# Kernel tuning notes

Measured on AMD Instinct MI355X. Metric: run time of the kernel, lower is better.

The kernel has to match this reference:

```python
import jax, jax.numpy as jnp
import numpy as np

K = 3       # kernel_size
STRIDE = 1


def setup_inputs() -> dict:
    key = jax.random.key(0)
    k1, k2, k3 = jax.random.split(key, 3)
    B, C, H, W = 128, 64, 32, 32
    O = 64
    OH = (H - K) // STRIDE + 1  # 30
    OW = (W - K) // STRIDE + 1  # 30
    x = jax.random.normal(k1, (B, C, H, W), dtype=jnp.float32)
    weight = jax.random.normal(k2, (O, C, OH, OW, K, K), dtype=jnp.float32)
    bias = jax.random.normal(k3, (O, OH, OW), dtype=jnp.float32)
    return {"x": x, "weight": weight, "bias": bias}


def reference(x, weight, bias):
    # x: [B, C, H, W]; weight: [O, C, OH, OW, K, K]; bias: [O, OH, OW]
    O, C, OH, OW, _, _ = weight.shape
    # Extract all k x k patches in one pass: [B, C*K*K, OH, OW],
    # feature axis ordered (C, kh, kw) with spatial fastest.
    patches = jax.lax.conv_general_dilated_patches(
        x, filter_shape=(K, K), window_strides=(STRIDE, STRIDE), padding="VALID"
    )
    # Faithful to torch einsum 'bcih,coih->bo': the region's channel axis is
    # contracted against the weight's FIRST axis (nominal out_channels), and the
    # output channel is the weight's SECOND axis (requires C == O).
    # Rearrange weight -> [C*K*K (contract), O (output), OH, OW].
    w = jnp.transpose(weight, (0, 4, 5, 1, 2, 3)).reshape(C * K * K, O, OH, OW)
    out = jnp.einsum("bpij,poij->boij", patches, w) + bias[None]
    return out  # [B, O, OH, OW]
```

## Files before the change

### kernel.cpp

```cpp
#include <hip/hip_runtime.h>


typedef __bf16 bf16x8 __attribute__((ext_vector_type(8)));
typedef float f32x4 __attribute__((ext_vector_type(4)));
typedef unsigned long long u64;
typedef unsigned int u32t;
typedef unsigned short u16t;

struct __attribute__((packed, aligned(8))) uf4 { f32x4 v; };
struct __attribute__((packed, aligned(8))) uf2 { float2 v; };
struct __attribute__((packed, aligned(4))) uq2 { u64 x, y; };
struct __attribute__((aligned(16))) ull2 { u64 x, y; };

__device__ __forceinline__ u16t f2bf(float f) {
  union { float f; u32t u; } v; v.f = f;
  u32t r = v.u + 0x7fffu + ((v.u >> 16) & 1u);
  return (u16t)(r >> 16);
}
__device__ __forceinline__ u32t pk2(float a, float b) {
  return (u32t)f2bf(a) | ((u32t)f2bf(b) << 16);
}
__device__ __forceinline__ u64 pk3(float a, float b, float c) {
  return (u64)f2bf(a) | ((u64)f2bf(b) << 16) | ((u64)f2bf(c) << 32);
}
__device__ __forceinline__ bf16x8 mk_af(u64 lo, u64 hi) {
  union { u64 q[2]; bf16x8 v; } u;
  u.q[0] = lo; u.q[1] = hi;
  return u.v;
}


__global__ __launch_bounds__(256) void lcl_prep_x(const float* __restrict__ x,
                                                  u16t* __restrict__ Xb) {
  int gid = blockIdx.x * 256 + threadIdx.x;
  int b  = gid & 127;
  int ch = gid >> 7;
  const float* src = x + (size_t)b * 65536 + ch * 32;
  u16t* dst = Xb + (size_t)gid * 32;
  u64 qv[8];
#pragma unroll
  for (int s = 0; s < 8; ++s) {
    f32x4 a = ((const uf4*)(src + s * 4))->v;
    qv[s] = (u64)pk2(a[0], a[1]) | ((u64)pk2(a[2], a[3]) << 32);
  }
#pragma unroll
  for (int s = 0; s < 4; ++s) {
    ull2 w; w.x = qv[2 * s]; w.y = qv[2 * s + 1];
    *(ull2*)(dst + s * 8) = w;
  }
}

__global__ __launch_bounds__(256, 2) void lcl_main(
    const u16t* __restrict__ Xb, const float* __restrict__ wgt,
    const float* __restrict__ bias, float* __restrict__ out) {
  int bid = blockIdx.x;
  int xcd = bid & 7, sg = bid >> 3;
  int t = xcd * 75 + sg;
  int jg = t % 5;
  int r  = t / 5;
  int bg = r & 1, og = (r >> 1) & 1, i = r >> 2;
  int j0 = jg * 6;
  int ij0 = i * 30 + j0;

  __shared__ __align__(16) u16t Bt[2 * 6 * 32 * 104];

  const int tid  = threadIdx.x;
  const int wave = tid >> 6;
  const int lane = tid & 63;
  const int lrow = lane & 15;
  const int q    = lane >> 4;

  const int b_x = bg * 64 + wave * 16 + lrow;
  const char* xbase = (const char*)Xb;
  u32t xoff[3][2];
#pragma unroll
  for (int s = 0; s < 3; ++s)
#pragma unroll
    for (int tt = 0; tt < 2; ++tt) {
      int g = s * 8 + q * 2 + tt, cc = g / 3, kh = g - cc * 3;
      xoff[s][tt] = (u32t)(((cc * 32 + (i + kh)) * 128 + b_x) * 64 + j0 * 2);
    }

  const int ccw = tid >> 5, ow = tid & 31;
  const float* wb = wgt + ((size_t)ccw * 64 + og * 32 + ow) * 8100 + ij0 * 9;

  uq2   rq[3][2];
  f32x4 wv[13];
  float2 wv2;

#define GF(K) ((K) < 52 ? wv[(K) >> 2][(K)&3] : ((K) == 52 ? wv2.x : wv2.y))

#define LOAD_CHUNK(C0)                                                      \
  {                                                                         \
    const size_t xadv = (size_t)(C0) * 262144;                              \
    _Pragma("unroll") for (int s = 0; s < 3; ++s)                           \
    _Pragma("unroll") for (int tt = 0; tt < 2; ++tt)                        \
      rq[s][tt] = *(const uq2*)(xbase + xadv + xoff[s][tt]);                \
    const float* wq = wb + (size_t)(C0) * 518400;                           \
    _Pragma("unroll") for (int e = 0; e < 13; ++e)                          \
      wv[e] = ((const uf4*)(wq + e * 4))->v;                                \
    wv2 = ((const uf2*)(wq + 52))->v;                                       \
  }

  f32x4 acc[6][2];
#pragma unroll
  for (int a = 0; a < 6; ++a)
#pragma unroll
    for (int n = 0; n < 2; ++n) acc[a][n] = f32x4{0.f, 0.f, 0.f, 0.f};

  LOAD_CHUNK(0)

  for (int chunk = 0; chunk < 8; ++chunk) {
    u16t* B = Bt + (chunk & 1) * 19968;

#pragma unroll
    for (int dj = 0; dj < 6; ++dj) {
      u16t* Bp = B + dj * 3328 + ow * 104 + ccw * 12;
#pragma unroll
      for (int kh = 0; kh < 3; ++kh) {
        const int k0 = dj * 9 + kh * 3;
        *(u64*)&Bp[kh * 4] = pk3(GF(k0), GF(k0 + 1), GF(k0 + 2));
      }
    }

    u64 rb[3][2][2];
#pragma unroll
    for (int s = 0; s < 3; ++s)
#pragma unroll
      for (int tt = 0; tt < 2; ++tt) {
        rb[s][tt][0] = rq[s][tt].x;
        rb[s][tt][1] = rq[s][tt].y;
      }

    __syncthreads();

    if (chunk < 7) LOAD_CHUNK((chunk + 1) * 8)

#pragma unroll
    for (int s = 0; s < 3; ++s) {
#pragma unroll
      for (int jj = 0; jj < 6; ++jj) {
        bf16x8 bfr0 = *(const bf16x8*)&B[jj * 3328 + lrow * 104 + s * 32 + q * 8];
        bf16x8 bfr1 = *(const bf16x8*)&B[jj * 3328 + (16 + lrow) * 104 + s * 32 + q * 8];
        u64 lo, hi;
        if (jj == 0) {
          lo = rb[s][0][0];
          hi = rb[s][1][0];
        } else if (jj < 4) {
          lo = (rb[s][0][0] >> (16 * jj)) | (rb[s][0][1] << (64 - 16 * jj));
          hi = (rb[s][1][0] >> (16 * jj)) | (rb[s][1][1] << (64 - 16 * jj));
        } else if (jj == 4) {
          lo = rb[s][0][1];
          hi = rb[s][1][1];
        } else {
          lo = rb[s][0][1] >> 16;
          hi = rb[s][1][1] >> 16;
        }
        bf16x8 af = mk_af(lo, hi);
        acc[jj][0] = __builtin_amdgcn_mfma_f32_16x16x32_bf16(af, bfr0, acc[jj][0], 0, 0, 0);
        acc[jj][1] = __builtin_amdgcn_mfma_f32_16x16x32_bf16(af, bfr1, acc[jj][1], 0, 0, 0);
      }
    }
  }

  const int b0 = bg * 64 + wave * 16 + q * 4;
#pragma unroll
  for (int nt = 0; nt < 2; ++nt) {
    int o = og * 32 + nt * 16 + lrow;
    const float* bp = bias + o * 900 + ij0;
    float2 bv0 = ((const uf2*)bp)->v;
    float2 bv1 = ((const uf2*)(bp + 2))->v;
    float2 bv2 = ((const uf2*)(bp + 4))->v;
#pragma unroll
    for (int rr = 0; rr < 4; ++rr) {
      float* op = out + (size_t)(b0 + rr) * 57600 + o * 900 + ij0;
      float2 r0{acc[0][nt][rr] + bv0.x, acc[1][nt][rr] + bv0.y};
      float2 r1{acc[2][nt][rr] + bv1.x, acc[3][nt][rr] + bv1.y};
      float2 r2{acc[4][nt][rr] + bv2.x, acc[5][nt][rr] + bv2.y};
      ((uf2*)op)->v = r0;
      ((uf2*)(op + 2))->v = r1;
      ((uf2*)(op + 4))->v = r2;
    }
  }
}

__global__ __launch_bounds__(256, 2) void lcl_r4(
    const float* __restrict__ x, const float* __restrict__ wgt,
    const float* __restrict__ bias, float* __restrict__ out) {
  int blk = blockIdx.x;
  int xcd = blk & 7, sg = blk >> 3;
  int t = xcd * 56 + (xcd < 2 ? xcd : 2) + sg;
  int i = t / 15;
  int j0 = (t % 15) * 2;
  int ij0 = i * 30 + j0;

  __shared__ __align__(16) u16t Bt[2 * 2 * 64 * 104];

  const int tid  = threadIdx.x;
  const int wave = tid >> 6;
  const int lane = tid & 63;
  const int lrow = lane & 15;
  const int q    = lane >> 4;

  {
    u64* zp = (u64*)Bt;
#pragma unroll
    for (int k = 0; k < 26; ++k) zp[tid + k * 256] = 0ull;
  }

  int xoffF[3][2];
#pragma unroll
  for (int s = 0; s < 3; ++s)
#pragma unroll
    for (int tt = 0; tt < 2; ++tt) {
      int g = s * 8 + q * 2 + tt, cc = g / 3, kh = g - cc * 3;
      xoffF[s][tt] = cc * 1024 + kh * 32;
    }
  const float* xb0 = x + (wave * 32 + lrow) * 65536 + i * 32 + j0;
  const float* xb1 = xb0 + 16 * 65536;

  const int o_w = tid & 63;
  const float* wb0 = wgt + (size_t)wave * 518400 + o_w * 8100 + ij0 * 9;
  const float* wb1 = wb0 + (size_t)4 * 518400;

  f32x4 av[2][3][2];
  f32x4 wv[2][5];

#define LOAD_CHUNK4(C0)                                                       \
  {                                                                           \
    const float* xc0 = xb0 + (C0) * 1024;                                     \
    const float* xc1 = xb1 + (C0) * 1024;                                     \
    _Pragma("unroll") for (int s = 0; s < 3; ++s)                             \
    _Pragma("unroll") for (int tt = 0; tt < 2; ++tt) {                        \
      av[0][s][tt] = ((const uf4*)(xc0 + xoffF[s][tt]))->v;                   \
      av[1][s][tt] = ((const uf4*)(xc1 + xoffF[s][tt]))->v;                   \
    }                                                                         \
    const float* w0 = wb0 + (size_t)(C0) * 518400;                            \
    const float* w1 = wb1 + (size_t)(C0) * 518400;                            \
    _Pragma("unroll") for (int e = 0; e < 4; ++e) {                           \
      wv[0][e] = ((const uf4*)(w0 + e * 4))->v;                               \
      wv[1][e] = ((const uf4*)(w1 + e * 4))->v;                               \
    }                                                                         \
    wv[0][4] = ((const uf4*)(w0 + 14))->v;                                    \
    wv[1][4] = ((const uf4*)(w1 + 14))->v;                                    \
  }

  f32x4 acc[2][2][4];
#pragma unroll
  for (int a = 0; a < 2; ++a)
#pragma unroll
    for (int b = 0; b < 2; ++b)
#pragma unroll
      for (int c = 0; c < 4; ++c) acc[a][b][c] = f32x4{0.f, 0.f, 0.f, 0.f};

  LOAD_CHUNK4(0)

  for (int chunk = 0; chunk < 8; ++chunk) {
    u16t* B = Bt + (chunk & 1) * 13312;
#pragma unroll
    for (int p = 0; p < 2; ++p) {
      int ccl = wave + 4 * p;
      u16t* Bp = B + o_w * 104 + ccl * 12;
      *(u32t*)&Bp[0] = pk2(wv[p][0][0], wv[p][0][1]);
      Bp[2]  = f2bf(wv[p][0][2]);
      Bp[4]  = f2bf(wv[p][0][3]);
      Bp[5]  = f2bf(wv[p][1][0]);
      Bp[6]  = f2bf(wv[p][1][1]);
      *(u32t*)&Bp[8] = pk2(wv[p][1][2], wv[p][1][3]);
      Bp[10] = f2bf(wv[p][2][0]);
      u16t* Bq = Bp + 6656;
      *(u32t*)&Bq[0] = pk2(wv[p][2][1], wv[p][2][2]);
      Bq[2]  = f2bf(wv[p][2][3]);
      Bq[4]  = f2bf(wv[p][3][0]);
      Bq[5]  = f2bf(wv[p][3][1]);
      Bq[6]  = f2bf(wv[p][3][2]);
      *(u32t*)&Bq[8] = pk2(wv[p][3][3], wv[p][4][2]);
      Bq[10] = f2bf(wv[p][4][3]);
    }

    u64 rb[2][3][2];
#pragma unroll
    for (int mt = 0; mt < 2; ++mt)
#pragma unroll
      for (int s = 0; s < 3; ++s)
#pragma unroll
        for (int tt = 0; tt < 2; ++tt) {
          const f32x4 vv = av[mt][s][tt];
          rb[mt][s][tt] = (u64)pk2(vv[0], vv[1]) | ((u64)pk2(vv[2], vv[3]) << 32);
        }

    __syncthreads();

    if (chunk < 7) LOAD_CHUNK4((chunk + 1) * 8)

#pragma unroll
    for (int s = 0; s < 3; ++s) {
      bf16x8 bfr[2][4];
#pragma unroll
      for (int jj = 0; jj < 2; ++jj)
#pragma unroll
        for (int nt = 0; nt < 4; ++nt)
          bfr[jj][nt] = *reinterpret_cast<const bf16x8*>(
              &B[jj * 6656 + (nt * 16 + lrow) * 104 + s * 32 + q * 8]);
#pragma unroll
      for (int mt = 0; mt < 2; ++mt)
#pragma unroll
        for (int jj = 0; jj < 2; ++jj) {
          u64 lo = rb[mt][s][0] >> (jj * 16);
          u64 hi = rb[mt][s][1] >> (jj * 16);
          bf16x8 af = mk_af(lo, hi);
#pragma unroll
          for (int nt = 0; nt < 4; ++nt)
            acc[mt][jj][nt] = __builtin_amdgcn_mfma_f32_16x16x32_bf16(
                af, bfr[jj][nt], acc[mt][jj][nt], 0, 0, 0);
        }
    }
  }

#pragma unroll
  for (int nt = 0; nt < 4; ++nt) {
    int o = nt * 16 + lrow;
    float2 bv = *(const float2*)(bias + o * 900 + ij0);
#pragma unroll
    for (int mt = 0; mt < 2; ++mt) {
#pragma unroll
      for (int rr = 0; rr < 4; ++rr) {
        int b = wave * 32 + mt * 16 + q * 4 + rr;
        float2 res;
        res.x = acc[mt][0][nt][rr] + bv.x;
        res.y = acc[mt][1][nt][rr] + bv.y;
        *(float2*)(out + b * 57600 + o * 900 + ij0) = res;
      }
    }
  }
}

extern "C" void kernel_launch(void* const* d_in, const int* in_sizes, int n_in,
                              void* d_out, int out_size, void* d_ws,
                              size_t ws_size, hipStream_t stream) {
  const float* x    = (const float*)d_in[0];
  const float* wgt  = (const float*)d_in[1];
  const float* bias = (const float*)d_in[2];
  float* out        = (float*)d_out;
  if (ws_size >= (size_t)16777216 && d_ws != nullptr) {
    lcl_prep_x<<<dim3(1024), dim3(256), 0, stream>>>(x, (u16t*)d_ws);
    lcl_main<<<dim3(600), dim3(256), 0, stream>>>((const u16t*)d_ws, wgt, bias, out);
  } else {
    lcl_r4<<<dim3(450), dim3(256), 0, stream>>>(x, wgt, bias, out);
  }
}
```

Measured before the change: 322.0 us.

## Remap weight loads so threads read contiguous 16B slices across channels

Changes the thread-to-weight mapping in the local-conv MFMA kernel. Each group of 8 threads now reads contiguous float4 slices of one output channel's 54-float weight run for 8 channels, instead of each thread reading a whole 54-float run. Each weight is scattered into shared memory as an individual bf16 store, and the shared tile is zeroed up front because some padding slots are no longer written. The epilogue also merges the bias loads and output stores into float4 plus float2 accesses. In exchange there are more LDS stores, unaligned 16B global loads and an extra zeroing pass.

```diff
diff --git a/kernel.cpp b/kernel.cpp
--- a/kernel.cpp
+++ b/kernel.cpp
@@ -8,6 +8,7 @@
 typedef unsigned short u16t;
 
 struct __attribute__((packed, aligned(8))) uf4 { f32x4 v; };
+struct __attribute__((packed, aligned(4))) uf4a { f32x4 v; };
 struct __attribute__((packed, aligned(8))) uf2 { float2 v; };
 struct __attribute__((packed, aligned(4))) uq2 { u64 x, y; };
 struct __attribute__((aligned(16))) ull2 { u64 x, y; };
@@ -19,9 +20,6 @@
 }
 __device__ __forceinline__ u32t pk2(float a, float b) {
   return (u32t)f2bf(a) | ((u32t)f2bf(b) << 16);
-}
-__device__ __forceinline__ u64 pk3(float a, float b, float c) {
-  return (u64)f2bf(a) | ((u64)f2bf(b) << 16) | ((u64)f2bf(c) << 32);
 }
 __device__ __forceinline__ bf16x8 mk_af(u64 lo, u64 hi) {
   union { u64 q[2]; bf16x8 v; } u;
@@ -70,6 +68,12 @@
   const int lrow = lane & 15;
   const int q    = lane >> 4;
 
+  {
+    u64* zp = (u64*)Bt;
+#pragma unroll
+    for (int k = 0; k < 39; ++k) zp[tid + k * 256] = 0ull;
+  }
+
   const int b_x = bg * 64 + wave * 16 + lrow;
   const char* xbase = (const char*)Xb;
   u32t xoff[3][2];
@@ -81,14 +85,20 @@
       xoff[s][tt] = (u32t)(((cc * 32 + (i + kh)) * 128 + b_x) * 64 + j0 * 2);
     }
 
-  const int ccw = tid >> 5, ow = tid & 31;
-  const float* wb = wgt + ((size_t)ccw * 64 + og * 32 + ow) * 8100 + ij0 * 9;
+  const int e8 = tid & 7, g8 = tid >> 3;
+  const int o_w = og * 32 + g8;
+  const int FO0 = e8 * 4;
+  const int FO1 = 22 + e8 * 4;
+  int Pofs[8];
+#pragma unroll
+  for (int jm = 0; jm < 8; ++jm) {
+    int F = ((jm & 4) ? FO1 : FO0) + (jm & 3);
+    Pofs[jm] = (F / 9) * 3328 + ((F % 9) / 3) * 4 + (F % 3);
+  }
+  const float* wb = wgt + (size_t)o_w * 8100 + ij0 * 9;
 
   uq2   rq[3][2];
-  f32x4 wv[13];
-  float2 wv2;
-
-#define GF(K) ((K) < 52 ? wv[(K) >> 2][(K)&3] : ((K) == 52 ? wv2.x : wv2.y))
+  f32x4 wreg[16];
 
 #define LOAD_CHUNK(C0)                                                      \
   {                                                                         \
@@ -96,10 +106,12 @@
     _Pragma("unroll") for (int s = 0; s < 3; ++s)                           \
     _Pragma("unroll") for (int tt = 0; tt < 2; ++tt)                        \
       rq[s][tt] = *(const uq2*)(xbase + xadv + xoff[s][tt]);                \
-    const float* wq = wb + (size_t)(C0) * 518400;                           \
-    _Pragma("unroll") for (int e = 0; e < 13; ++e)                          \
-      wv[e] = ((const uf4*)(wq + e * 4))->v;                                \
-    wv2 = ((const uf2*)(wq + 52))->v;                                       \
+    _Pragma("unroll") for (int k = 0; k < 16; ++k) {                        \
+      const int p_ = k >> 1;                                                \
+      const float* wq = wb + (size_t)((C0) + p_) * 518400 +                 \
+                        ((k & 1) ? FO1 : FO0);                              \
+      wreg[k] = ((const uf4a*)wq)->v;                                       \
+    }                                                                       \
   }
 
   f32x4 acc[6][2];
@@ -109,18 +121,16 @@
     for (int n = 0; n < 2; ++n) acc[a][n] = f32x4{0.f, 0.f, 0.f, 0.f};
 
   LOAD_CHUNK(0)
+  __syncthreads();
 
   for (int chunk = 0; chunk < 8; ++chunk) {
-    u16t* B = Bt + (chunk & 1) * 19968;
-
-#pragma unroll
-    for (int dj = 0; dj < 6; ++dj) {
-      u16t* Bp = B + dj * 3328 + ow * 104 + ccw * 12;
-#pragma unroll
-      for (int kh = 0; kh < 3; ++kh) {
-        const int k0 = dj * 9 + kh * 3;
-        *(u64*)&Bp[kh * 4] = pk3(GF(k0), GF(k0 + 1), GF(k0 + 2));
-      }
+    u16t* Bb = Bt + (chunk & 1) * 19968 + g8 * 104;
+#pragma unroll
+    for (int k = 0; k < 16; ++k) {
+      const int p_ = k >> 1, h_ = k & 1;
+#pragma unroll
+      for (int m = 0; m < 4; ++m)
+        (Bb + Pofs[h_ * 4 + m])[p_ * 12] = f2bf(wreg[k][m]);
     }
 
     u64 rb[3][2][2];
@@ -140,8 +150,10 @@
     for (int s = 0; s < 3; ++s) {
 #pragma unroll
       for (int jj = 0; jj < 6; ++jj) {
-        bf16x8 bfr0 = *(const bf16x8*)&B[jj * 3328 + lrow * 104 + s * 32 + q * 8];
-        bf16x8 bfr1 = *(const bf16x8*)&B[jj * 3328 + (16 + lrow) * 104 + s * 32 + q * 8];
+        bf16x8 bfr0 = *(const bf16x8*)&Bt[(chunk & 1) * 19968 + jj * 3328 +
+                                          lrow * 104 + s * 32 + q * 8];
+        bf16x8 bfr1 = *(const bf16x8*)&Bt[(chunk & 1) * 19968 + jj * 3328 +
+                                          (16 + lrow) * 104 + s * 32 + q * 8];
         u64 lo, hi;
         if (jj == 0) {
           lo = rb[s][0][0];
@@ -168,18 +180,21 @@
   for (int nt = 0; nt < 2; ++nt) {
     int o = og * 32 + nt * 16 + lrow;
     const float* bp = bias + o * 900 + ij0;
-    float2 bv0 = ((const uf2*)bp)->v;
-    float2 bv1 = ((const uf2*)(bp + 2))->v;
-    float2 bv2 = ((const uf2*)(bp + 4))->v;
+    f32x4 b03 = ((const uf4*)bp)->v;
+    float2 b45 = ((const uf2*)(bp + 4))->v;
 #pragma unroll
     for (int rr = 0; rr < 4; ++rr) {
       float* op = out + (size_t)(b0 + rr) * 57600 + o * 900 + ij0;
-      float2 r0{acc[0][nt][rr] + bv0.x, acc[1][nt][rr] + bv0.y};
-      float2 r1{acc[2][nt][rr] + bv1.x, acc[3][nt][rr] + bv1.y};
-      float2 r2{acc[4][nt][rr] + bv2.x, acc[5][nt][rr] + bv2.y};
-      ((uf2*)op)->v = r0;
-      ((uf2*)(op + 2))->v = r1;
-      ((uf2*)(op + 4))->v = r2;
+      f32x4 r03;
+      r03[0] = acc[0][nt][rr] + b03[0];
+      r03[1] = acc[1][nt][rr] + b03[1];
+      r03[2] = acc[2][nt][rr] + b03[2];
+      r03[3] = acc[3][nt][rr] + b03[3];
+      float2 r45;
+      r45.x = acc[4][nt][rr] + b45.x;
+      r45.y = acc[5][nt][rr] + b45.y;
+      ((uf4*)op)->v = r03;
+      ((uf2*)(op + 4))->v = r45;
     }
   }
 }
```

After: 284.4 us. 1.13x faster.
